# Kernel tuning notes

Measured on AMD Instinct MI355X. Metric: run time of the kernel, lower is better.

Reference implementation:

```python
import jax, jax.numpy as jnp
import numpy as np

N_EMBD = 2048
EXPAND = 2
D_INNER = N_EMBD * EXPAND          # 4096
D_STATE = 128
N_HEADS = D_INNER // D_STATE       # 32
HEAD_DIM = D_INNER // N_HEADS      # 128
N_GROUPS = 1
D_CONV = 4
CHUNK = 64
N_LAYERS = 48
GS = N_GROUPS * D_STATE
PROJ = 2 * D_INNER + N_HEADS + 2 * GS  # 8480
RMS_EPS = 1e-6


def _ssd_scan(A, B, C, dt, x, chunk_size=CHUNK):
    """Mamba-2 SSD chunked selective scan. A:(b,t,h) B,C:(b,t,g,n) dt:(b,t,h) x:(b,t,h,p)."""
    batch, seq_len, n_heads, P = x.shape
    G, N = B.shape[2], B.shape[3]
    Hg = n_heads // G
    Q = chunk_size
    pad_len = -seq_len % Q
    if pad_len:
        A = jnp.pad(A, ((0, 0), (0, pad_len), (0, 0)))
        B = jnp.pad(B, ((0, 0), (0, pad_len), (0, 0), (0, 0)))
        C = jnp.pad(C, ((0, 0), (0, pad_len), (0, 0), (0, 0)))
        dt = jnp.pad(dt, ((0, 0), (0, pad_len), (0, 0)))
        x = jnp.pad(x, ((0, 0), (0, pad_len), (0, 0), (0, 0)))
    T_pad = seq_len + pad_len
    n_chunks = T_pad // Q
    A_c = A.reshape(batch, n_chunks, Q, n_heads)
    B_c = B.reshape(batch, n_chunks, Q, G, N)
    C_c = C.reshape(batch, n_chunks, Q, G, N)
    dt_c = dt.reshape(batch, n_chunks, Q, n_heads)
    x_c = x.reshape(batch, n_chunks, Q, n_heads, P)
    log_a = A_c * dt_c
    cum_log_a = jnp.cumsum(log_a, axis=2)
    chunk_log_decay = cum_log_a[:, :, -1, :]
    log_diff = cum_log_a[:, :, :, None, :] - cum_log_a[:, :, None, :, :]
    causal = jnp.tril(jnp.ones((Q, Q), dtype=jnp.bool_))[None, None, :, :, None]
    L = jnp.exp(jnp.where(causal, log_diff, -jnp.inf))
    CB = jnp.einsum('bcign,bcjgn->bcijg', C_c, B_c)
    L_rs = L.reshape(batch, n_chunks, Q, Q, G, Hg)
    dt_rs = dt_c.reshape(batch, n_chunks, Q, G, Hg)
    x_rs = x_c.reshape(batch, n_chunks, Q, G, Hg, P)
    y_intra = jnp.einsum('bcijGH,bcijG,bcjGH,bcjGHp->bciGHp', L_rs, CB, dt_rs, x_rs)
    decay_to_end = jnp.exp(chunk_log_decay[:, :, None, :] - cum_log_a)
    decay_to_end_rs = decay_to_end.reshape(batch, n_chunks, Q, G, Hg)
    state_local = jnp.einsum('bcjGH,bcjGH,bcjGn,bcjGHp->bcGHnp', decay_to_end_rs, dt_rs, B_c, x_rs)
    chunk_decay = jnp.exp(chunk_log_decay).reshape(batch, n_chunks, G, Hg)

    def scan_op(left, right):
        d_l, s_l = left
        d_r, s_r = right
        return (d_l * d_r, d_r[..., None, None] * s_l + s_r)

    _, state_at_end = jax.lax.associative_scan(scan_op, (chunk_decay, state_local), axis=1)
    state_at_start = jnp.concatenate([jnp.zeros_like(state_at_end[:, :1]), state_at_end[:, :-1]], axis=1)
    decay_from_start = jnp.exp(cum_log_a).reshape(batch, n_chunks, Q, G, Hg)
    y_inter = jnp.einsum('bciGH,bciGn,bcGHnp->bciGHp', decay_from_start, C_c, state_at_start)
    y = (y_intra + y_inter).reshape(batch, T_pad, n_heads, P)
    if pad_len:
        y = y[:, :seq_len]
    return y


def setup_inputs() -> dict:
    key = jax.random.key(0)
    ks = jax.random.split(key, 6)
    Bsz, T = 2, 2048
    x = jax.random.normal(ks[0], (Bsz, T, N_EMBD), jnp.float32)
    norm_scale = jnp.ones((N_EMBD,), jnp.float32)
    in_proj_w = 0.02 * jax.random.normal(ks[1], (N_EMBD, PROJ), jnp.float32)
    conv_weight = 0.02 * jax.random.normal(ks[2], (D_CONV, D_INNER), jnp.float32)
    conv_bias = jnp.zeros((D_INNER,), jnp.float32)
    A_log = jnp.log(jnp.arange(1, N_HEADS + 1, dtype=jnp.float32))
    dt_bias = 0.1 * jax.random.normal(ks[3], (N_HEADS,), jnp.float32)
    D = jnp.ones((D_INNER,), jnp.float32)
    out_proj_w = (0.02 / np.sqrt(2 * N_LAYERS)) * jax.random.normal(ks[4], (D_INNER, N_EMBD), jnp.float32)
    return dict(x=x, norm_scale=norm_scale, in_proj_w=in_proj_w, conv_weight=conv_weight,
                conv_bias=conv_bias, A_log=A_log, dt_bias=dt_bias, D=D, out_proj_w=out_proj_w)


def reference(x, norm_scale, in_proj_w, conv_weight, conv_bias, A_log, dt_bias, D, out_proj_w):
    residual = x
    b, t = x.shape[0], x.shape[1]
    # RMSNorm
    h = x * jax.lax.rsqrt(jnp.mean(x * x, axis=-1, keepdims=True) + RMS_EPS) * norm_scale
    proj = h @ in_proj_w  # (b, t, PROJ)
    gate = proj[..., :D_INNER]
    ssm_in = proj[..., D_INNER:2 * D_INNER]
    dt_raw = proj[..., 2 * D_INNER:2 * D_INNER + N_HEADS]
    Bm = proj[..., 2 * D_INNER + N_HEADS:2 * D_INNER + N_HEADS + GS].reshape(b, t, N_GROUPS, D_STATE)
    Cm = proj[..., 2 * D_INNER + N_HEADS + GS:].reshape(b, t, N_GROUPS, D_STATE)
    # causal depthwise short conv
    xp = jnp.pad(ssm_in, ((0, 0), (D_CONV - 1, 0), (0, 0)))
    w_t = conv_weight.T[:, None, :]  # (D_INNER, 1, D_CONV)
    y = jax.lax.conv_general_dilated(jnp.transpose(xp, (0, 2, 1)), w_t,
                                     window_strides=(1,), padding='VALID',
                                     feature_group_count=D_INNER)
    ssm_in = jnp.transpose(y, (0, 2, 1)) + conv_bias
    ssm_in = jax.nn.silu(ssm_in)
    dt = jax.nn.softplus(dt_raw + dt_bias)
    A = -jnp.exp(A_log)
    A_f = jnp.broadcast_to(A[None, None, :], (b, t, N_HEADS))
    x_h = ssm_in.reshape(b, t, N_HEADS, HEAD_DIM)
    y_ssd = _ssd_scan(A_f, Bm, Cm, dt, x_h).reshape(b, t, D_INNER)
    y_ssd = y_ssd + D * ssm_in
    y_ssd = y_ssd * jax.nn.silu(gate)
    return residual + y_ssd @ out_proj_w
```

## Files before the change

### kernel.cpp

```cpp
#include <hip/hip_runtime.h>

typedef unsigned short u16;
typedef unsigned short u16x8 __attribute__((ext_vector_type(8)));
typedef __bf16 bf16x8 __attribute__((ext_vector_type(8)));
typedef float f32x4 __attribute__((ext_vector_type(4)));


__device__ __forceinline__ float bf2f(u16 u) {
    union { unsigned int i; float f; } v; v.i = ((unsigned int)u) << 16; return v.f;
}
__device__ __forceinline__ u16 f2bf(float f) {
    unsigned int u = __float_as_uint(f);
    u += 0x7fffu + ((u >> 16) & 1u);
    return (u16)(u >> 16);
}
__device__ __forceinline__ bf16x8 ld8(const u16* p) {
    return __builtin_bit_cast(bf16x8, *reinterpret_cast<const u16x8*>(p));
}
__device__ __forceinline__ void load_lds16(const u16* g, u16* l) {
    __builtin_amdgcn_global_load_lds(
        (const __attribute__((address_space(1))) unsigned int*)g,
        (__attribute__((address_space(3))) unsigned int*)l, 16, 0, 0);
}
__device__ __forceinline__ float fexp(float x) { return __expf(x); }
__device__ __forceinline__ float frcp(float x) { return __builtin_amdgcn_rcpf(x); }

__global__ __launch_bounds__(256) void k_rmsnorm(const float* __restrict__ x,
                                                 const float* __restrict__ scale,
                                                 u16* __restrict__ h) {
    int row = blockIdx.x, tid = threadIdx.x;
    const float4* xr = reinterpret_cast<const float4*>(x + (size_t)row * 2048);
    float4 v0 = xr[tid], v1 = xr[tid + 256];
    float ss = v0.x*v0.x + v0.y*v0.y + v0.z*v0.z + v0.w*v0.w
             + v1.x*v1.x + v1.y*v1.y + v1.z*v1.z + v1.w*v1.w;
#pragma unroll
    for (int off = 32; off > 0; off >>= 1) ss += __shfl_down(ss, off, 64);
    __shared__ float red[4];
    if ((tid & 63) == 0) red[tid >> 6] = ss;
    __syncthreads();
    float r = rsqrtf((red[0] + red[1] + red[2] + red[3]) * (1.f / 2048.f) + 1e-6f);
    const float4* sc = reinterpret_cast<const float4*>(scale);
    float4 s0 = sc[tid], s1 = sc[tid + 256];
    ushort4 o0, o1;
    o0.x = f2bf(v0.x * r * s0.x); o0.y = f2bf(v0.y * r * s0.y);
    o0.z = f2bf(v0.z * r * s0.z); o0.w = f2bf(v0.w * r * s0.w);
    o1.x = f2bf(v1.x * r * s1.x); o1.y = f2bf(v1.y * r * s1.y);
    o1.z = f2bf(v1.z * r * s1.z); o1.w = f2bf(v1.w * r * s1.w);
    ushort4* hr = reinterpret_cast<ushort4*>(h + (size_t)row * 2048);
    hr[tid] = o0; hr[tid + 256] = o1;
}

__global__ __launch_bounds__(256) void k_wcast(const float* __restrict__ W,
                                               u16* __restrict__ Wt,
                                               int K, int N) {
    __shared__ u16 Ts[64][72];
    int n0 = blockIdx.x * 64, k0 = blockIdx.y * 64;
    int t = threadIdx.x;
    int jl = (t & 15) * 4;
#pragma unroll
    for (int s = 0; s < 4; ++s) {
        int kl = s * 16 + (t >> 4);
        if (n0 + jl + 4 <= N) {
            float4 v = *reinterpret_cast<const float4*>(W + (size_t)(k0 + kl) * N + n0 + jl);
            Ts[kl][jl] = f2bf(v.x); Ts[kl][jl + 1] = f2bf(v.y);
            Ts[kl][jl + 2] = f2bf(v.z); Ts[kl][jl + 3] = f2bf(v.w);
        } else {
#pragma unroll
            for (int e = 0; e < 4; ++e)
                Ts[kl][jl + e] = (n0 + jl + e < N) ? f2bf(W[(size_t)(k0 + kl) * N + n0 + jl + e]) : (u16)0;
        }
    }
    __syncthreads();
    int nl = t >> 2, kl0 = (t & 3) * 16;
    u16 tmp[16];
#pragma unroll
    for (int e = 0; e < 16; ++e) tmp[e] = Ts[kl0 + e][nl];
    u16* dst = Wt + (size_t)(n0 + nl) * K + k0 + kl0;
    *reinterpret_cast<uint4*>(dst) = *reinterpret_cast<uint4*>(tmp);
    *reinterpret_cast<uint4*>(dst + 8) = *reinterpret_cast<uint4*>(tmp + 8);
}

template <bool BF16_OUT, int MAP>
__global__ __launch_bounds__(256) void k_gemm128(const u16* __restrict__ A,
                                                 const u16* __restrict__ Bt,
                                                 u16* __restrict__ Cb,
                                                 float* __restrict__ Cf,
                                                 const float* __restrict__ resid,
                                                 int M, int Nw, int ldc, int ncoff,
                                                 int K, int nbt) {
    __shared__ u16 As[8192];
    __shared__ u16 Bs[8192];
    int bid = blockIdx.x;
    int mb, nb;
    if (MAP == 0) {
        int mt = M >> 7;
        int grp = mt * 8;
        int g = bid / grp, l = bid % grp;
        nb = g * 8 + (l & 7); mb = l >> 3;
        if (nb * 128 >= Nw) return;
    } else {
        nb = bid % nbt; mb = bid / nbt;
    }
    int m0 = mb * 128, n0 = nb * 128;

    int t = threadIdx.x, lane = t & 63, w = t >> 6;
    int row = t >> 2, kc = (t & 3) * 8;
    int wm = (w >> 1) * 64, wn = (w & 1) * 64;
    int r = lane & 15, q = lane >> 4;

    f32x4 acc[4][4];
#pragma unroll
    for (int a = 0; a < 4; ++a)
#pragma unroll
        for (int b = 0; b < 4; ++b) acc[a][b] = (f32x4){0.f, 0.f, 0.f, 0.f};

    const u16* ga0 = A + (size_t)(m0 + row) * K + kc;
    const u16* ga1 = A + (size_t)(m0 + 64 + row) * K + kc;
    const u16* gb0 = Bt + (size_t)(ncoff + n0 + row) * K + kc;
    const u16* gb1 = Bt + (size_t)(ncoff + n0 + 64 + row) * K + kc;

    for (int k0 = 0; k0 < K; k0 += 64) {
        load_lds16(ga0 + k0,      As + w * 512);
        load_lds16(ga1 + k0,      As + 2048 + w * 512);
        load_lds16(gb0 + k0,      Bs + w * 512);
        load_lds16(gb1 + k0,      Bs + 2048 + w * 512);
        load_lds16(ga0 + k0 + 32, As + 4096 + w * 512);
        load_lds16(ga1 + k0 + 32, As + 4096 + 2048 + w * 512);
        load_lds16(gb0 + k0 + 32, Bs + 4096 + w * 512);
        load_lds16(gb1 + k0 + 32, Bs + 4096 + 2048 + w * 512);
        __syncthreads();
#pragma unroll
        for (int h = 0; h < 2; ++h) {
            bf16x8 af[4], bf[4];
#pragma unroll
            for (int mi = 0; mi < 4; ++mi) af[mi] = ld8(&As[h * 4096 + (wm + mi * 16 + r) * 32 + q * 8]);
#pragma unroll
            for (int ni = 0; ni < 4; ++ni) bf[ni] = ld8(&Bs[h * 4096 + (wn + ni * 16 + r) * 32 + q * 8]);
#pragma unroll
            for (int mi = 0; mi < 4; ++mi)
#pragma unroll
                for (int ni = 0; ni < 4; ++ni)
                    acc[mi][ni] = __builtin_amdgcn_mfma_f32_16x16x32_bf16(af[mi], bf[ni], acc[mi][ni], 0, 0, 0);
        }
        __syncthreads();
    }
#pragma unroll
    for (int mi = 0; mi < 4; ++mi)
#pragma unroll
        for (int ni = 0; ni < 4; ++ni) {
            int lgn = n0 + wn + ni * 16 + r;
            if (lgn < Nw) {
#pragma unroll
                for (int rg = 0; rg < 4; ++rg) {
                    int gm = m0 + wm + mi * 16 + q * 4 + rg;
                    float vv = acc[mi][ni][rg];
                    if (BF16_OUT) {
                        Cb[(size_t)gm * ldc + ncoff + lgn] = f2bf(vv);
                    } else {
                        if (resid) vv += resid[(size_t)gm * ldc + ncoff + lgn];
                        Cf[(size_t)gm * ldc + ncoff + lgn] = vv;
                    }
                }
            }
        }
}

__global__ __launch_bounds__(512, 2) void k_gemm256(const u16* __restrict__ A,
                                                    const u16* __restrict__ Bt,
                                                    u16* __restrict__ C,
                                                    int M, int Nout, int ldc, int K) {
    __shared__ u16 lds[65536];
    const int nkt = K >> 6;
    int mt = M >> 8;
    int bid = blockIdx.x;
    int swz = (bid & 7) * ((int)gridDim.x >> 3) + (bid >> 3);
    int mb = swz % mt, nb = swz / mt;
    int m0 = mb << 8, n0 = nb << 8;

    int t = threadIdx.x;
    int ln = t & 63, w = t >> 6;
    int wm = w >> 2, wn = w & 3;
    int r = ln & 15, q = ln >> 4;
    int xq = (q << 3) ^ ((r & 7) << 3);

    int rr = ln >> 3;
    int cc8 = ((ln & 7) ^ rr) << 3;
    const u16* Ag = A + (size_t)(m0 + w * 8 + rr) * K + cc8;
    const u16* Bg = Bt + (size_t)(n0 + w * 8 + rr) * K + cc8;
    u16* ldsw = lds + (w << 9);
    const size_t K64 = (size_t)K * 64;
    const size_t K128 = (size_t)K * 128;

    f32x4 acc[8][4];
#pragma unroll
    for (int a = 0; a < 8; ++a)
#pragma unroll
        for (int b = 0; b < 4; ++b) acc[a][b] = (f32x4){0.f, 0.f, 0.f, 0.f};

    auto stageA = [&](int ti, int h) {
        if (ti >= nkt) return;
        const u16* g = Ag + ((size_t)ti << 6) + (h ? K128 : (size_t)0);
        u16* d = ldsw + ((ti & 1) << 14) + (h << 13);
        load_lds16(g, d);
        load_lds16(g + K64, d + 4096);
    };
    auto stageB = [&](int ti, int h) {
        if (ti >= nkt) return;
        const u16* g = Bg + ((size_t)ti << 6) + (h ? K128 : (size_t)0);
        u16* d = ldsw + 32768 + ((ti & 1) << 14) + (h << 13);
        load_lds16(g, d);
        load_lds16(g + K64, d + 4096);
    };

    stageA(0, 0); stageB(0, 0); stageB(0, 1); stageA(0, 1);
    stageA(1, 0); stageB(1, 0); stageB(1, 1);
    asm volatile("s_waitcnt vmcnt(6)" ::: "memory");
    __builtin_amdgcn_s_barrier();
    asm volatile("" ::: "memory");

    bf16x8 aF[4][2], bLo[2][2], bHi[2][2];

    for (int kt = 0; kt < nkt; ++kt) {
        const u16* Ah = lds + ((kt & 1) << 14) + (wm << 13);
        const u16* Bh = lds + 32768 + ((kt & 1) << 14) + ((wn >> 1) << 13) + ((wn & 1) << 12);

#pragma unroll
        for (int mi = 0; mi < 4; ++mi)
#pragma unroll
            for (int ks = 0; ks < 2; ++ks)
                aF[mi][ks] = ld8(Ah + (mi * 16 + r) * 64 + (xq ^ (ks << 5)));
#pragma unroll
        for (int ni = 0; ni < 2; ++ni)
#pragma unroll
            for (int ks = 0; ks < 2; ++ks)
                bLo[ni][ks] = ld8(Bh + (ni * 16 + r) * 64 + (xq ^ (ks << 5)));
        stageA(kt + 1, 1);
        asm volatile("" ::: "memory");
        __builtin_amdgcn_s_barrier();
        asm volatile("s_waitcnt lgkmcnt(0)" ::: "memory");
        __builtin_amdgcn_s_setprio(1);
#pragma unroll
        for (int mi = 0; mi < 4; ++mi)
#pragma unroll
            for (int ni = 0; ni < 2; ++ni)
#pragma unroll
                for (int ks = 0; ks < 2; ++ks)
                    acc[mi][ni] = __builtin_amdgcn_mfma_f32_16x16x32_bf16(aF[mi][ks], bLo[ni][ks], acc[mi][ni], 0, 0, 0);
        __builtin_amdgcn_s_setprio(0);
        asm volatile("" ::: "memory");
        __builtin_amdgcn_s_barrier();
        asm volatile("" ::: "memory");

#pragma unroll
        for (int ni = 0; ni < 2; ++ni)
#pragma unroll
            for (int ks = 0; ks < 2; ++ks)
                bHi[ni][ks] = ld8(Bh + ((ni + 2) * 16 + r) * 64 + (xq ^ (ks << 5)));
        asm volatile("" ::: "memory");
        __builtin_amdgcn_s_barrier();
        asm volatile("s_waitcnt lgkmcnt(0)" ::: "memory");
        __builtin_amdgcn_s_setprio(1);
#pragma unroll
        for (int mi = 0; mi < 4; ++mi)
#pragma unroll
            for (int ni = 0; ni < 2; ++ni)
#pragma unroll
                for (int ks = 0; ks < 2; ++ks)
                    acc[mi][ni + 2] = __builtin_amdgcn_mfma_f32_16x16x32_bf16(aF[mi][ks], bHi[ni][ks], acc[mi][ni + 2], 0, 0, 0);
        __builtin_amdgcn_s_setprio(0);
        asm volatile("" ::: "memory");
        __builtin_amdgcn_s_barrier();
        asm volatile("" ::: "memory");

#pragma unroll
        for (int mi = 0; mi < 4; ++mi)
#pragma unroll
            for (int ks = 0; ks < 2; ++ks)
                aF[mi][ks] = ld8(Ah + ((mi + 4) * 16 + r) * 64 + (xq ^ (ks << 5)));
        stageB(kt + 2, 0);
        asm volatile("" ::: "memory");
        __builtin_amdgcn_s_barrier();
        asm volatile("s_waitcnt lgkmcnt(0)" ::: "memory");
        __builtin_amdgcn_s_setprio(1);
#pragma unroll
        for (int mi = 0; mi < 4; ++mi)
#pragma unroll
            for (int ni = 0; ni < 2; ++ni)
#pragma unroll
                for (int ks = 0; ks < 2; ++ks)
                    acc[mi + 4][ni + 2] = __builtin_amdgcn_mfma_f32_16x16x32_bf16(aF[mi][ks], bHi[ni][ks], acc[mi + 4][ni + 2], 0, 0, 0);
        __builtin_amdgcn_s_setprio(0);
        asm volatile("" ::: "memory");
        __builtin_amdgcn_s_barrier();
        asm volatile("" ::: "memory");

        stageB(kt + 2, 1);
        stageA(kt + 2, 0);
        asm volatile("" ::: "memory");
        __builtin_amdgcn_s_barrier();
        __builtin_amdgcn_s_setprio(1);
#pragma unroll
        for (int mi = 0; mi < 4; ++mi)
#pragma unroll
            for (int ni = 0; ni < 2; ++ni)
#pragma unroll
                for (int ks = 0; ks < 2; ++ks)
                    acc[mi + 4][ni] = __builtin_amdgcn_mfma_f32_16x16x32_bf16(aF[mi][ks], bLo[ni][ks], acc[mi + 4][ni], 0, 0, 0);
        __builtin_amdgcn_s_setprio(0);
        if (kt + 2 < nkt) { asm volatile("s_waitcnt vmcnt(6)" ::: "memory"); }
        else              { asm volatile("s_waitcnt vmcnt(0)" ::: "memory"); }
        __builtin_amdgcn_s_barrier();
        asm volatile("" ::: "memory");
    }

#pragma unroll
    for (int mi = 0; mi < 8; ++mi)
#pragma unroll
        for (int ni = 0; ni < 4; ++ni) {
            int gn = n0 + wn * 64 + ni * 16 + r;
            if (gn < Nout) {
#pragma unroll
                for (int rg = 0; rg < 4; ++rg) {
                    int gm = m0 + wm * 128 + mi * 16 + q * 4 + rg;
                    C[(size_t)gm * ldc + gn] = f2bf(acc[mi][ni][rg]);
                }
            }
        }
}

__global__ __launch_bounds__(64) void k_dt(const u16* __restrict__ proj,
                                           const float* __restrict__ A_log,
                                           const float* __restrict__ dt_bias,
                                           float* __restrict__ dt,
                                           float* __restrict__ cumla) {
    int bid = blockIdx.x;
    int b = bid >> 10, hh = (bid >> 5) & 31, c = bid & 31;
    int j = threadIdx.x;
    int t = c * 64 + j;
    float z = bf2f(proj[(size_t)(b * 2048 + t) * 8480 + 8192 + hh]) + dt_bias[hh];
    float dtv = (z > 20.f) ? z : log1pf(fexp(z));
    float v = -fexp(A_log[hh]) * dtv;
#pragma unroll
    for (int off = 1; off < 64; off <<= 1) {
        float pv = __shfl_up(v, off, 64);
        if (j >= off) v += pv;
    }
    int base = ((b * 32 + hh) * 32 + c) * 64;
    dt[base + j] = dtv;
    cumla[base + j] = v;
}

__global__ __launch_bounds__(256) void k_intra(const u16* __restrict__ proj,
                                               const float* __restrict__ dt,
                                               const float* __restrict__ cumla,
                                               const float* __restrict__ cw,
                                               const float* __restrict__ cb,
                                               const float* __restrict__ Dv,
                                               u16* __restrict__ ybuf,
                                               u16* __restrict__ states) {
    __shared__ u16 Xt[128][72];
    __shared__ u16 Bt[128][72];
    __shared__ union {
        u16 Ms[64][72];
        struct { float cwl[4][128]; float cbl[128]; } cv;
    } sh;
    __shared__ float dts[64], clas[64];
    int bid = blockIdx.x;
    int b = bid >> 10, c = (bid >> 5) & 31, hh = bid & 31;
    int tid = threadIdx.x, lane = tid & 63, w = tid >> 6;
    int r = lane & 15, q = lane >> 4;
    int t0 = b * 2048 + c * 64;
    int sbase = ((b * 32 + hh) * 32 + c) * 64;

    if (tid < 64) { dts[tid] = dt[sbase + tid]; clas[tid] = cumla[sbase + tid]; }
    if (tid < 128) {
        sh.cv.cbl[tid] = cb[hh * 128 + tid];
#pragma unroll
        for (int k = 0; k < 4; ++k) sh.cv.cwl[k][tid] = cw[k * 4096 + hh * 128 + tid];
    }
    __syncthreads();

    {
        int j = tid & 63;
        float wj = fexp(clas[63] - clas[j]) * dts[j];
        for (int g = tid >> 6; g < 16; g += 4) {
            int p0 = g * 8;
            u16 tb[8];
            *reinterpret_cast<uint4*>(tb) =
                *reinterpret_cast<const uint4*>(proj + (size_t)(t0 + j) * 8480 + 8224 + p0);
            float xv[8];
#pragma unroll
            for (int e = 0; e < 8; ++e) xv[e] = sh.cv.cbl[p0 + e];
#pragma unroll
            for (int kk = 0; kk < 4; ++kk) {
                int tl = c * 64 + j - 3 + kk;
                if (tl >= 0) {
                    u16 srow[8];
                    *reinterpret_cast<uint4*>(srow) =
                        *reinterpret_cast<const uint4*>(proj + (size_t)(b * 2048 + tl) * 8480 + 4096 + hh * 128 + p0);
#pragma unroll
                    for (int e = 0; e < 8; ++e) xv[e] += sh.cv.cwl[kk][p0 + e] * bf2f(srow[e]);
                }
            }
#pragma unroll
            for (int e = 0; e < 8; ++e) {
                float s = xv[e] * frcp(1.f + fexp(-xv[e]));
                Xt[p0 + e][j] = f2bf(s);
                Bt[p0 + e][j] = f2bf(wj * bf2f(tb[e]));
            }
        }
    }
    __syncthreads();

    {
        const u16* crow = proj + (size_t)(t0 + w * 16 + r) * 8480 + 8352;
        bf16x8 af[4];
#pragma unroll
        for (int k = 0; k < 4; ++k) af[k] = ld8(crow + k * 32 + q * 8);
#pragma unroll
        for (int tj = 0; tj < 4; ++tj) {
            const u16* brow = proj + (size_t)(t0 + tj * 16 + r) * 8480 + 8224;
            f32x4 acc = (f32x4){0.f, 0.f, 0.f, 0.f};
#pragma unroll
            for (int k = 0; k < 4; ++k)
                acc = __builtin_amdgcn_mfma_f32_16x16x32_bf16(af[k], ld8(brow + k * 32 + q * 8), acc, 0, 0, 0);
            int j = tj * 16 + r;
            float dj = dts[j], cj = clas[j];
#pragma unroll
            for (int rg = 0; rg < 4; ++rg) {
                int i = w * 16 + q * 4 + rg;
                float m = (j <= i) ? acc[rg] * fexp(clas[i] - cj) * dj : 0.f;
                sh.Ms[i][j] = f2bf(m);
            }
        }
    }
    __syncthreads();

    {
        bf16x8 af[2];
#pragma unroll
        for (int k = 0; k < 2; ++k) af[k] = ld8(&sh.Ms[w * 16 + r][k * 32 + q * 8]);
#pragma unroll
        for (int tj = 0; tj < 8; ++tj) {
            f32x4 acc = (f32x4){0.f, 0.f, 0.f, 0.f};
#pragma unroll
            for (int k = 0; k < 2; ++k)
                acc = __builtin_amdgcn_mfma_f32_16x16x32_bf16(af[k], ld8(&Xt[tj * 16 + r][k * 32 + q * 8]), acc, 0, 0, 0);
            int p = tj * 16 + r;
            float dv = Dv[hh * 128 + p];
#pragma unroll
            for (int rg = 0; rg < 4; ++rg) {
                int i = w * 16 + q * 4 + rg;
                float v = acc[rg] + dv * bf2f(Xt[p][i]);
                ybuf[(size_t)(t0 + i) * 4096 + hh * 128 + p] = f2bf(v);
            }
        }
    }

    size_t sb = ((size_t)((b * 32 + hh) * 32 + c)) * 16384;
#pragma unroll
    for (int th = 0; th < 2; ++th) {
        int ti = w + th * 4;
        bf16x8 af[2];
#pragma unroll
        for (int k = 0; k < 2; ++k) af[k] = ld8(&Xt[ti * 16 + r][k * 32 + q * 8]);
#pragma unroll
        for (int tj = 0; tj < 8; ++tj) {
            f32x4 acc = (f32x4){0.f, 0.f, 0.f, 0.f};
#pragma unroll
            for (int k = 0; k < 2; ++k)
                acc = __builtin_amdgcn_mfma_f32_16x16x32_bf16(af[k], ld8(&Bt[tj * 16 + r][k * 32 + q * 8]), acc, 0, 0, 0);
            int n = tj * 16 + r;
#pragma unroll
            for (int rg = 0; rg < 4; ++rg) {
                int p = ti * 16 + q * 4 + rg;
                states[sb + p * 128 + n] = f2bf(acc[rg]);
            }
        }
    }
}

__global__ __launch_bounds__(256) void k_scan(u16* __restrict__ states,
                                              const float* __restrict__ cumla) {
    int gid = blockIdx.x * 256 + threadIdx.x;
    int bh = gid >> 12;
    int q4 = (gid & 4095) * 4;
    size_t base = (size_t)bh * 32 * 16384 + q4;
    float s0 = 0.f, s1 = 0.f, s2 = 0.f, s3 = 0.f;
    for (int c = 0; c < 32; ++c) {
        float cd = fexp(cumla[(bh * 32 + c) * 64 + 63]);
        size_t idx = base + (size_t)c * 16384;
        ushort4 v = *reinterpret_cast<ushort4*>(states + idx);
        float l0 = bf2f(v.x), l1 = bf2f(v.y), l2 = bf2f(v.z), l3 = bf2f(v.w);
        ushort4 o; o.x = f2bf(s0); o.y = f2bf(s1); o.z = f2bf(s2); o.w = f2bf(s3);
        *reinterpret_cast<ushort4*>(states + idx) = o;
        s0 = cd * s0 + l0; s1 = cd * s1 + l1; s2 = cd * s2 + l2; s3 = cd * s3 + l3;
    }
}

__global__ __launch_bounds__(256) void k_inter(const u16* __restrict__ proj,
                                               const u16* __restrict__ states,
                                               const float* __restrict__ cumla,
                                               const u16* __restrict__ ybuf,
                                               u16* __restrict__ ygated) {
    __shared__ u16 Ss[128][136];
    __shared__ float clav[64];
    int bid = blockIdx.x;
    int b = bid >> 10, c = (bid >> 5) & 31, hh = bid & 31;
    int tid = threadIdx.x, lane = tid & 63, w = tid >> 6;
    int r = lane & 15, q = lane >> 4;
    int t0 = b * 2048 + c * 64;
    int sbase = ((b * 32 + hh) * 32 + c) * 64;
    size_t sb = ((size_t)((b * 32 + hh) * 32 + c)) * 16384;

    if (tid < 64) clav[tid] = fexp(cumla[sbase + tid]);
    for (int e = tid; e < 2048; e += 256) {
        int p = e >> 4, n8 = (e & 15) * 8;
        *reinterpret_cast<uint4*>(&Ss[p][n8]) =
            *reinterpret_cast<const uint4*>(states + sb + p * 128 + n8);
    }
    __syncthreads();

    const u16* crow = proj + (size_t)(t0 + w * 16 + r) * 8480 + 8352;
    bf16x8 af[4];
#pragma unroll
    for (int k = 0; k < 4; ++k) af[k] = ld8(crow + k * 32 + q * 8);
#pragma unroll
    for (int tj = 0; tj < 8; ++tj) {
        f32x4 acc = (f32x4){0.f, 0.f, 0.f, 0.f};
#pragma unroll
        for (int k = 0; k < 4; ++k)
            acc = __builtin_amdgcn_mfma_f32_16x16x32_bf16(af[k], ld8(&Ss[tj * 16 + r][k * 32 + q * 8]), acc, 0, 0, 0);
        int p = tj * 16 + r;
        int ch = hh * 128 + p;
#pragma unroll
        for (int rg = 0; rg < 4; ++rg) {
            int i = w * 16 + q * 4 + rg;
            size_t td = (size_t)(t0 + i) * 4096 + ch;
            float v = clav[i] * acc[rg] + bf2f(ybuf[td]);
            float g = bf2f(proj[(size_t)(t0 + i) * 8480 + ch]);
            ygated[td] = f2bf(v * (g * frcp(1.f + fexp(-g))));
        }
    }
}

extern "C" void kernel_launch(void* const* d_in, const int* in_sizes, int n_in,
                              void* d_out, int out_size, void* d_ws, size_t ws_size,
                              hipStream_t stream) {
    const float* x          = (const float*)d_in[0];
    const float* norm_scale = (const float*)d_in[1];
    const float* in_proj_w  = (const float*)d_in[2];
    const float* conv_w     = (const float*)d_in[3];
    const float* conv_b     = (const float*)d_in[4];
    const float* A_log      = (const float*)d_in[5];
    const float* dt_bias    = (const float*)d_in[6];
    const float* Dv         = (const float*)d_in[7];
    const float* out_w      = (const float*)d_in[8];
    float* out = (float*)d_out;

    char* ws = (char*)d_ws;
    u16*   states = (u16*)(ws);
    u16*   h      = (u16*)(ws);
    u16*   wbt    = (u16*)(ws + 16777216);
    u16*   proj   = (u16*)(ws + 67108864);
    u16*   owt    = (u16*)(ws + 136577024);
    u16*   ybuf   = (u16*)(ws + 170131456);
    float* dt     = (float*)(ws + 203685888);
    float* cumla  = (float*)(ws + 204210176);

    k_rmsnorm<<<4096, 256, 0, stream>>>(x, norm_scale, h);
    k_wcast<<<dim3(136, 32), 256, 0, stream>>>(in_proj_w, wbt, 2048, 8480);
    k_gemm128<true, 1><<<96, 256, 0, stream>>>(h, wbt, proj, nullptr, nullptr,
                                               4096, 288, 8480, 8192, 2048, 3);
    k_gemm256<<<512, 512, 0, stream>>>(h, wbt, proj, 4096, 8192, 8480, 2048);
    k_dt<<<2048, 64, 0, stream>>>(proj, A_log, dt_bias, dt, cumla);
    k_intra<<<2048, 256, 0, stream>>>(proj, dt, cumla, conv_w, conv_b, Dv, ybuf, states);
    k_scan<<<1024, 256, 0, stream>>>(states, cumla);
    k_inter<<<2048, 256, 0, stream>>>(proj, states, cumla, ybuf, ybuf);
    k_wcast<<<dim3(32, 64), 256, 0, stream>>>(out_w, owt, 4096, 2048);
    k_gemm128<false, 0><<<512, 256, 0, stream>>>(ybuf, owt, nullptr, out, x,
                                                 4096, 2048, 2048, 0, 4096, 16);
}
```

Before: 569.5 us.

## Use split-K 256-tile GEMM for output projection with separate residual reduction

The output projection moves from the 128-tile GEMM to the 256-tile kernel. K is split in two, each half writes fp32 partials to workspace, and a new kernel adds the two partials plus the residual x. This gives 256 blocks on the large-tile MFMA pipeline instead of 512 smaller tiles. The main loop's global-to-LDS staging order also changes: A and B halves are issued together, one barrier is dropped, and the vmcnt waits are adjusted. The cost is extra fp32 partial traffic (two 32MB buffers), an extra launch, and the risk that the altered staging order races or stalls in the input-projection GEMM.

```diff
diff --git a/kernel.cpp b/kernel.cpp
--- a/kernel.cpp
+++ b/kernel.cpp
@@ -165,17 +165,23 @@
         }
 }
 
+template <bool F32OUT>
 __global__ __launch_bounds__(512, 2) void k_gemm256(const u16* __restrict__ A,
                                                     const u16* __restrict__ Bt,
-                                                    u16* __restrict__ C,
-                                                    int M, int Nout, int ldc, int K) {
+                                                    u16* __restrict__ Cb,
+                                                    float* __restrict__ Cf,
+                                                    int M, int Nout, int ldc,
+                                                    int lda, int Kl) {
     __shared__ u16 lds[65536];
-    const int nkt = K >> 6;
+    const int nkt = Kl >> 6;
     int mt = M >> 8;
     int bid = blockIdx.x;
     int swz = (bid & 7) * ((int)gridDim.x >> 3) + (bid >> 3);
-    int mb = swz % mt, nb = swz / mt;
+    int tiles = mt * (Nout >> 8);
+    int tp = swz % tiles, ks = swz / tiles;
+    int mb = tp % mt, nb = tp / mt;
     int m0 = mb << 8, n0 = nb << 8;
+    int koff = ks * Kl;
 
     int t = threadIdx.x;
     int ln = t & 63, w = t >> 6;
@@ -185,11 +191,11 @@
 
     int rr = ln >> 3;
     int cc8 = ((ln & 7) ^ rr) << 3;
-    const u16* Ag = A + (size_t)(m0 + w * 8 + rr) * K + cc8;
-    const u16* Bg = Bt + (size_t)(n0 + w * 8 + rr) * K + cc8;
+    const u16* Ag = A + (size_t)(m0 + w * 8 + rr) * lda + koff + cc8;
+    const u16* Bg = Bt + (size_t)(n0 + w * 8 + rr) * lda + koff + cc8;
     u16* ldsw = lds + (w << 9);
-    const size_t K64 = (size_t)K * 64;
-    const size_t K128 = (size_t)K * 128;
+    const size_t R64 = (size_t)lda * 64;
+    const size_t R128 = (size_t)lda * 128;
 
     f32x4 acc[8][4];
 #pragma unroll
@@ -199,22 +205,22 @@
 
     auto stageA = [&](int ti, int h) {
         if (ti >= nkt) return;
-        const u16* g = Ag + ((size_t)ti << 6) + (h ? K128 : (size_t)0);
+        const u16* g = Ag + ((size_t)ti << 6) + (h ? R128 : (size_t)0);
         u16* d = ldsw + ((ti & 1) << 14) + (h << 13);
         load_lds16(g, d);
-        load_lds16(g + K64, d + 4096);
+        load_lds16(g + R64, d + 4096);
     };
     auto stageB = [&](int ti, int h) {
         if (ti >= nkt) return;
-        const u16* g = Bg + ((size_t)ti << 6) + (h ? K128 : (size_t)0);
+        const u16* g = Bg + ((size_t)ti << 6) + (h ? R128 : (size_t)0);
         u16* d = ldsw + 32768 + ((ti & 1) << 14) + (h << 13);
         load_lds16(g, d);
-        load_lds16(g + K64, d + 4096);
+        load_lds16(g + R64, d + 4096);
     };
 
-    stageA(0, 0); stageB(0, 0); stageB(0, 1); stageA(0, 1);
-    stageA(1, 0); stageB(1, 0); stageB(1, 1);
-    asm volatile("s_waitcnt vmcnt(6)" ::: "memory");
+    stageA(0, 0); stageA(0, 1); stageB(0, 0); stageB(0, 1);
+    stageA(1, 0); stageA(1, 1); stageB(1, 0); stageB(1, 1);
+    asm volatile("s_waitcnt vmcnt(8)" ::: "memory");
     __builtin_amdgcn_s_barrier();
     asm volatile("" ::: "memory");
 
@@ -227,14 +233,13 @@
 #pragma unroll
         for (int mi = 0; mi < 4; ++mi)
 #pragma unroll
-            for (int ks = 0; ks < 2; ++ks)
-                aF[mi][ks] = ld8(Ah + (mi * 16 + r) * 64 + (xq ^ (ks << 5)));
+            for (int ks2 = 0; ks2 < 2; ++ks2)
+                aF[mi][ks2] = ld8(Ah + (mi * 16 + r) * 64 + (xq ^ (ks2 << 5)));
 #pragma unroll
         for (int ni = 0; ni < 2; ++ni)
 #pragma unroll
-            for (int ks = 0; ks < 2; ++ks)
-                bLo[ni][ks] = ld8(Bh + (ni * 16 + r) * 64 + (xq ^ (ks << 5)));
-        stageA(kt + 1, 1);
+            for (int ks2 = 0; ks2 < 2; ++ks2)
+                bLo[ni][ks2] = ld8(Bh + (ni * 16 + r) * 64 + (xq ^ (ks2 << 5)));
         asm volatile("" ::: "memory");
         __builtin_amdgcn_s_barrier();
         asm volatile("s_waitcnt lgkmcnt(0)" ::: "memory");
@@ -244,8 +249,8 @@
 #pragma unroll
             for (int ni = 0; ni < 2; ++ni)
 #pragma unroll
-                for (int ks = 0; ks < 2; ++ks)
-                    acc[mi][ni] = __builtin_amdgcn_mfma_f32_16x16x32_bf16(aF[mi][ks], bLo[ni][ks], acc[mi][ni], 0, 0, 0);
+                for (int ks2 = 0; ks2 < 2; ++ks2)
+                    acc[mi][ni] = __builtin_amdgcn_mfma_f32_16x16x32_bf16(aF[mi][ks2], bLo[ni][ks2], acc[mi][ni], 0, 0, 0);
         __builtin_amdgcn_s_setprio(0);
         asm volatile("" ::: "memory");
         __builtin_amdgcn_s_barrier();
@@ -254,8 +259,8 @@
 #pragma unroll
         for (int ni = 0; ni < 2; ++ni)
 #pragma unroll
-            for (int ks = 0; ks < 2; ++ks)
-                bHi[ni][ks] = ld8(Bh + ((ni + 2) * 16 + r) * 64 + (xq ^ (ks << 5)));
+            for (int ks2 = 0; ks2 < 2; ++ks2)
+                bHi[ni][ks2] = ld8(Bh + ((ni + 2) * 16 + r) * 64 + (xq ^ (ks2 << 5)));
         asm volatile("" ::: "memory");
         __builtin_amdgcn_s_barrier();
         asm volatile("s_waitcnt lgkmcnt(0)" ::: "memory");
@@ -265,8 +270,8 @@
 #pragma unroll
             for (int ni = 0; ni < 2; ++ni)
 #pragma unroll
-                for (int ks = 0; ks < 2; ++ks)
-                    acc[mi][ni + 2] = __builtin_amdgcn_mfma_f32_16x16x32_bf16(aF[mi][ks], bHi[ni][ks], acc[mi][ni + 2], 0, 0, 0);
+                for (int ks2 = 0; ks2 < 2; ++ks2)
+                    acc[mi][ni + 2] = __builtin_amdgcn_mfma_f32_16x16x32_bf16(aF[mi][ks2], bHi[ni][ks2], acc[mi][ni + 2], 0, 0, 0);
         __builtin_amdgcn_s_setprio(0);
         asm volatile("" ::: "memory");
         __builtin_amdgcn_s_barrier();
@@ -275,9 +280,10 @@
 #pragma unroll
         for (int mi = 0; mi < 4; ++mi)
 #pragma unroll
-            for (int ks = 0; ks < 2; ++ks)
-                aF[mi][ks] = ld8(Ah + ((mi + 4) * 16 + r) * 64 + (xq ^ (ks << 5)));
+            for (int ks2 = 0; ks2 < 2; ++ks2)
+                aF[mi][ks2] = ld8(Ah + ((mi + 4) * 16 + r) * 64 + (xq ^ (ks2 << 5)));
         stageB(kt + 2, 0);
+        stageB(kt + 2, 1);
         asm volatile("" ::: "memory");
         __builtin_amdgcn_s_barrier();
         asm volatile("s_waitcnt lgkmcnt(0)" ::: "memory");
@@ -287,27 +293,25 @@
 #pragma unroll
             for (int ni = 0; ni < 2; ++ni)
 #pragma unroll
-                for (int ks = 0; ks < 2; ++ks)
-                    acc[mi + 4][ni + 2] = __builtin_amdgcn_mfma_f32_16x16x32_bf16(aF[mi][ks], bHi[ni][ks], acc[mi + 4][ni + 2], 0, 0, 0);
+                for (int ks2 = 0; ks2 < 2; ++ks2)
+                    acc[mi + 4][ni + 2] = __builtin_amdgcn_mfma_f32_16x16x32_bf16(aF[mi][ks2], bHi[ni][ks2], acc[mi + 4][ni + 2], 0, 0, 0);
         __builtin_amdgcn_s_setprio(0);
         asm volatile("" ::: "memory");
         __builtin_amdgcn_s_barrier();
         asm volatile("" ::: "memory");
 
-        stageB(kt + 2, 1);
         stageA(kt + 2, 0);
-        asm volatile("" ::: "memory");
-        __builtin_amdgcn_s_barrier();
+        stageA(kt + 2, 1);
         __builtin_amdgcn_s_setprio(1);
 #pragma unroll
         for (int mi = 0; mi < 4; ++mi)
 #pragma unroll
             for (int ni = 0; ni < 2; ++ni)
 #pragma unroll
-                for (int ks = 0; ks < 2; ++ks)
-                    acc[mi + 4][ni] = __builtin_amdgcn_mfma_f32_16x16x32_bf16(aF[mi][ks], bLo[ni][ks], acc[mi + 4][ni], 0, 0, 0);
+                for (int ks2 = 0; ks2 < 2; ++ks2)
+                    acc[mi + 4][ni] = __builtin_amdgcn_mfma_f32_16x16x32_bf16(aF[mi][ks2], bLo[ni][ks2], acc[mi + 4][ni], 0, 0, 0);
         __builtin_amdgcn_s_setprio(0);
-        if (kt + 2 < nkt) { asm volatile("s_waitcnt vmcnt(6)" ::: "memory"); }
+        if (kt + 2 < nkt) { asm volatile("s_waitcnt vmcnt(8)" ::: "memory"); }
         else              { asm volatile("s_waitcnt vmcnt(0)" ::: "memory"); }
         __builtin_amdgcn_s_barrier();
         asm volatile("" ::: "memory");
@@ -322,10 +326,31 @@
 #pragma unroll
                 for (int rg = 0; rg < 4; ++rg) {
                     int gm = m0 + wm * 128 + mi * 16 + q * 4 + rg;
-                    C[(size_t)gm * ldc + gn] = f2bf(acc[mi][ni][rg]);
+                    if (F32OUT) {
+                        Cf[(size_t)ks * M * Nout + (size_t)gm * Nout + gn] = acc[mi][ni][rg];
+                    } else {
+                        Cb[(size_t)gm * ldc + gn] = f2bf(acc[mi][ni][rg]);
+                    }
                 }
             }
         }
+}
+
+__global__ __launch_bounds__(256) void k_addred(const float* __restrict__ x,
+                                                const float* __restrict__ P0,
+                                                const float* __restrict__ P1,
+                                                float* __restrict__ out) {
+    const float4* xv = reinterpret_cast<const float4*>(x);
+    const float4* a = reinterpret_cast<const float4*>(P0);
+    const float4* b = reinterpret_cast<const float4*>(P1);
+    float4* o = reinterpret_cast<float4*>(out);
+    for (int k = blockIdx.x * 256 + threadIdx.x; k < 2097152; k += 524288) {
+        float4 xx = xv[k], aa = a[k], bb = b[k];
+        float4 r;
+        r.x = xx.x + aa.x + bb.x; r.y = xx.y + aa.y + bb.y;
+        r.z = xx.z + aa.z + bb.z; r.w = xx.w + aa.w + bb.w;
+        o[k] = r;
+    }
 }
 
 __global__ __launch_bounds__(64) void k_dt(const u16* __restrict__ proj,
@@ -562,6 +587,7 @@
     u16*   states = (u16*)(ws);
     u16*   h      = (u16*)(ws);
     u16*   wbt    = (u16*)(ws + 16777216);
+    float* parts  = (float*)(ws);
     u16*   proj   = (u16*)(ws + 67108864);
     u16*   owt    = (u16*)(ws + 136577024);
     u16*   ybuf   = (u16*)(ws + 170131456);
@@ -572,12 +598,14 @@
     k_wcast<<<dim3(136, 32), 256, 0, stream>>>(in_proj_w, wbt, 2048, 8480);
     k_gemm128<true, 1><<<96, 256, 0, stream>>>(h, wbt, proj, nullptr, nullptr,
                                                4096, 288, 8480, 8192, 2048, 3);
-    k_gemm256<<<512, 512, 0, stream>>>(h, wbt, proj, 4096, 8192, 8480, 2048);
+    k_gemm256<false><<<512, 512, 0, stream>>>(h, wbt, proj, nullptr,
+                                              4096, 8192, 8480, 2048, 2048);
     k_dt<<<2048, 64, 0, stream>>>(proj, A_log, dt_bias, dt, cumla);
     k_intra<<<2048, 256, 0, stream>>>(proj, dt, cumla, conv_w, conv_b, Dv, ybuf, states);
     k_scan<<<1024, 256, 0, stream>>>(states, cumla);
     k_inter<<<2048, 256, 0, stream>>>(proj, states, cumla, ybuf, ybuf);
     k_wcast<<<dim3(32, 64), 256, 0, stream>>>(out_w, owt, 4096, 2048);
-    k_gemm128<false, 0><<<512, 256, 0, stream>>>(ybuf, owt, nullptr, out, x,
-                                                 4096, 2048, 2048, 0, 4096, 16);
-}
+    k_gemm256<true><<<256, 512, 0, stream>>>(ybuf, owt, nullptr, parts,
+                                             4096, 2048, 2048, 4096, 2048);
+    k_addred<<<2048, 256, 0, stream>>>(x, parts, parts + 8388608, out);
+}
```

Measured after the change: 548.0 us. 3.8% less time.
